# Performance work log

Hardware: AMD Instinct MI355X
Metric: run time of the kernel (lower is better)

Reference implementation:

```python
import jax, jax.numpy as jnp
import numpy as np

SLOPE = 25.0  # fast_sigmoid surrogate slope
BETA = 0.5    # leaky membrane decay

@jax.custom_vjp
def spike_fn(v):
    # heaviside(v) with fast_sigmoid surrogate gradient; v = mem - threshold
    return (v > 0).astype(v.dtype)

def _spike_fwd(v):
    return (v > 0).astype(v.dtype), v

def _spike_bwd(v, g):
    return (g / (SLOPE * jnp.abs(v) + 1.0) ** 2,)

spike_fn.defvjp(_spike_fwd, _spike_bwd)

def _snn_forward(x, Ws, thrs, num_steps):
    # x: [B, T, IN] (time_first=False) -> [T, B, IN]
    xt = jnp.transpose(x, (1, 0, 2))[:num_steps]
    B = x.shape[0]
    mems0 = tuple(jnp.zeros((B, W.shape[0]), x.dtype) for W in Ws)

    def step(mems, x_t):
        spk = x_t
        new = []
        for W, thr, m in zip(Ws, thrs, mems):
            cur = spk @ W.T  # Linear, bias=False (dropout = identity in eval mode)
            # snntorch Leaky, reset_mechanism='subtract': reset computed from
            # previous mem and detached (mem_reset), then mem = beta*mem + I - reset*thr
            reset = jax.lax.stop_gradient((m > thr).astype(cur.dtype))
            m = BETA * m + cur - reset * thr
            spk = spike_fn(m - thr)
            new.append(m)
        return tuple(new), (spk, new[-1])

    _, (spk_rec, mem_rec) = jax.lax.scan(step, mems0, xt)
    return spk_rec, mem_rec  # each [T, B, OUT]

def setup_inputs() -> dict:
    key = jax.random.key(0)
    ks = jax.random.split(key, 4)
    B, T, IN, H, OUT = 256, 100, 700, 1024, 20
    x = jax.random.uniform(ks[0], (B, T, IN), dtype=jnp.float32)
    s0 = 1.0 / np.sqrt(IN)
    s1 = 1.0 / np.sqrt(H)
    W0 = jax.random.uniform(ks[1], (H, IN), jnp.float32, -s0, s0)
    W1 = jax.random.uniform(ks[2], (H, H), jnp.float32, -s1, s1)
    W2 = jax.random.uniform(ks[3], (OUT, H), jnp.float32, -s1, s1)
    thr = jnp.float32(0.1)
    return {"x": x, "W0": W0, "W1": W1, "W2": W2,
            "thr0": thr, "thr1": thr, "thr2": thr, "num_steps": T}

def reference(x, W0, W1, W2, thr0, thr1, thr2, num_steps):
    return _snn_forward(x, (W0, W1, W2), (thr0, thr1, thr2), num_steps)
```

## Files before the change

kernel.cpp:

```cpp
#include <hip/hip_runtime.h>
#include <hip/hip_bf16.h>
#include <stdint.h>

#define BATCH   256
#define T_STEPS 100
#define IN_DIM  700
#define H_DIM   1024
#define OUT_DIM 20
#define TC      8
#define NCHUNK  13


__device__ __forceinline__ void lif_epilogue8(
    const float s[4][4], float thr,
    float* __restrict__ mstate, uint16_t* __restrict__ spk_bits,
    int b, int n0, int tbase, int tx, int ty, int ln)
{
    const int half = ty & 1;
    const int g = ty & 3;
    float m[4];
#pragma unroll
    for (int j = 0; j < 4; ++j)
        m[j] = mstate[(size_t)b * H_DIM + n0 + tx + 16 * j];
#pragma unroll
    for (int i = 0; i < 4; ++i) {
#pragma unroll
        for (int j = 0; j < 4; ++j) {
            const float rst = (m[j] > thr) ? thr : 0.f;
            float v = 0.5f * m[j] + s[i][j];
            v = v - rst; m[j] = v;
        }
        const int t = tbase + i;
#pragma unroll
        for (int j = 0; j < 4; ++j) {
            const unsigned long long mask = __ballot(m[j] > thr);
            if (tx == 0 && half == 0 && t < T_STEPS)
                spk_bits[((size_t)t * BATCH + b) * 64 + (n0 >> 4) + j] =
                    (uint16_t)((mask >> (16 * g)) & 0xFFFFull);
        }
    }
#pragma unroll
    for (int j = 0; j < 4; ++j)
        m[j] = __shfl(m[j], half ? (ln - 16) : ln);
#pragma unroll
    for (int i = 0; i < 4; ++i) {
#pragma unroll
        for (int j = 0; j < 4; ++j) {
            const float rst = (m[j] > thr) ? thr : 0.f;
            float v = 0.5f * m[j] + s[i][j];
            v = v - rst; m[j] = v;
        }
        const int t = tbase + 4 + i;
#pragma unroll
        for (int j = 0; j < 4; ++j) {
            const unsigned long long mask = __ballot(m[j] > thr);
            if (tx == 0 && half == 1 && t < T_STEPS)
                spk_bits[((size_t)t * BATCH + b) * 64 + (n0 >> 4) + j] =
                    (uint16_t)((mask >> (16 * g)) & 0xFFFFull);
        }
    }
    if (half == 1) {
#pragma unroll
        for (int j = 0; j < 4; ++j)
            mstate[(size_t)b * H_DIM + n0 + tx + 16 * j] = m[j];
    }
}

__global__ __launch_bounds__(256, 4) void fused_l0_l1(
    const float* __restrict__ x,
    const float* __restrict__ W0,
    const float* __restrict__ W1,
    const float* __restrict__ thr0_p,
    const float* __restrict__ thr1_p,
    float* __restrict__ m0state,
    float* __restrict__ m1state,
    uint16_t* __restrict__ spk0_bits,
    uint16_t* __restrict__ spk1_bits,
    int tc)
{
    __shared__ __align__(16) float As[64][68];
    __shared__ __align__(16) float Ws[64][68];

    const int tid = threadIdx.x;
    const int tx = tid & 15, ty = tid >> 4, ln = tid & 63;
    const int by = blockIdx.y;
    const bool isL0 = (blockIdx.x < 16);
    const int n0 = (isL0 ? blockIdx.x : blockIdx.x - 16) * 64;
    const int myc = isL0 ? tc : tc - 1;
    if (isL0 && myc >= NCHUNK) return;
    if (!isL0 && myc < 0) return;

    float ps[4][4], s[4][4];
#pragma unroll
    for (int i = 0; i < 4; ++i)
#pragma unroll
        for (int j = 0; j < 4; ++j) { ps[i][j] = 0.f; s[i][j] = 0.f; }

    const int sr = tid >> 2, q4 = tid & 3;
    const int b_s = 8 * by + (sr >> 3);
    int t_s = myc * TC + (sr & 7);
    if (t_s > T_STEPS - 1) t_s = T_STEPS - 1;
    const int b = 8 * by + (ty >> 1);

    if (isL0) {
        const float* xsrc = x + ((size_t)b_s * T_STEPS + t_s) * IN_DIM;
        const float* wsrc = W0 + (size_t)(n0 + sr) * IN_DIM;
#pragma unroll 1
        for (int c = 0; c < 11; ++c) {
            __syncthreads();
#pragma unroll
            for (int u = 0; u < 4; ++u) {
                const int f4 = q4 * 4 + u;
                const int k = c * 64 + f4 * 4;
                const float4 av = (k < IN_DIM) ? *(const float4*)(xsrc + k)
                                               : make_float4(0.f, 0.f, 0.f, 0.f);
                *(float4*)&As[sr][f4 * 4] = av;
                const float4 wv = (k < IN_DIM) ? *(const float4*)(wsrc + k)
                                               : make_float4(0.f, 0.f, 0.f, 0.f);
                *(float4*)&Ws[sr][f4 * 4] = wv;
            }
            __syncthreads();
            const int kmax4 = (c == 10) ? 15 : 16;
            for (int k4 = 0; k4 < kmax4; ++k4) {
                float4 av[4], wv[4];
#pragma unroll
                for (int i = 0; i < 4; ++i)
                    av[i] = *(const float4*)&As[4 * ty + i][k4 * 4];
#pragma unroll
                for (int j = 0; j < 4; ++j)
                    wv[j] = *(const float4*)&Ws[tx + 16 * j][k4 * 4];
#pragma unroll
                for (int i = 0; i < 4; ++i)
#pragma unroll
                    for (int j = 0; j < 4; ++j) {
                        ps[i][j] = __builtin_fmaf(av[i].x, wv[j].x, ps[i][j]);
                        ps[i][j] = __builtin_fmaf(av[i].y, wv[j].y, ps[i][j]);
                        ps[i][j] = __builtin_fmaf(av[i].z, wv[j].z, ps[i][j]);
                        ps[i][j] = __builtin_fmaf(av[i].w, wv[j].w, ps[i][j]);
                    }
            }
            if (c == 7 || c == 10) {
#pragma unroll
                for (int i = 0; i < 4; ++i)
#pragma unroll
                    for (int j = 0; j < 4; ++j) { s[i][j] += ps[i][j]; ps[i][j] = 0.f; }
            }
        }
        lif_epilogue8(s, *thr0_p, m0state, spk0_bits, b, n0, myc * TC, tx, ty, ln);
    } else {
        const uint16_t* bsrc = spk0_bits + ((size_t)t_s * BATCH + b_s) * 64;
        const float* wsrc = W1 + (size_t)(n0 + sr) * H_DIM;
#pragma unroll 1
        for (int c = 0; c < 16; ++c) {
            __syncthreads();
            {
                const uint32_t w = bsrc[c * 4 + q4];
#pragma unroll
                for (int u = 0; u < 4; ++u) {
                    float4 v;
                    v.x = ((w >> (u * 4 + 0)) & 1u) ? 1.0f : 0.0f;
                    v.y = ((w >> (u * 4 + 1)) & 1u) ? 1.0f : 0.0f;
                    v.z = ((w >> (u * 4 + 2)) & 1u) ? 1.0f : 0.0f;
                    v.w = ((w >> (u * 4 + 3)) & 1u) ? 1.0f : 0.0f;
                    *(float4*)&As[sr][(q4 * 4 + u) * 4] = v;
                }
#pragma unroll
                for (int u = 0; u < 4; ++u) {
                    const int f4 = q4 * 4 + u;
                    const float4 wv = *(const float4*)(wsrc + c * 64 + f4 * 4);
                    *(float4*)&Ws[sr][f4 * 4] = wv;
                }
            }
            __syncthreads();
            for (int k4 = 0; k4 < 16; ++k4) {
                float4 av[4], wv[4];
#pragma unroll
                for (int i = 0; i < 4; ++i)
                    av[i] = *(const float4*)&As[4 * ty + i][k4 * 4];
#pragma unroll
                for (int j = 0; j < 4; ++j)
                    wv[j] = *(const float4*)&Ws[tx + 16 * j][k4 * 4];
#pragma unroll
                for (int i = 0; i < 4; ++i)
#pragma unroll
                    for (int j = 0; j < 4; ++j) {
                        ps[i][j] = __builtin_fmaf(av[i].x, wv[j].x, ps[i][j]);
                        ps[i][j] = __builtin_fmaf(av[i].y, wv[j].y, ps[i][j]);
                        ps[i][j] = __builtin_fmaf(av[i].z, wv[j].z, ps[i][j]);
                        ps[i][j] = __builtin_fmaf(av[i].w, wv[j].w, ps[i][j]);
                    }
            }
            if (c == 7 || c == 15) {
#pragma unroll
                for (int i = 0; i < 4; ++i)
#pragma unroll
                    for (int j = 0; j < 4; ++j) { s[i][j] += ps[i][j]; ps[i][j] = 0.f; }
            }
        }
        lif_epilogue8(s, *thr1_p, m1state, spk1_bits, b, n0, myc * TC, tx, ty, ln);
    }
}

__global__ __launch_bounds__(256) void k2a_gemm(
    const uint16_t* __restrict__ spk1_bits,
    const float* __restrict__ W2,
    float* __restrict__ cur2h)
{
    const int gid = blockIdx.x * 256 + threadIdx.x;
    const int grp = gid / 25600;
    const int q   = gid % 25600;
    const int nq  = grp >> 1;
    const int h   = grp & 1;

    const uint16_t* bits = spk1_bits + (size_t)q * 64 + h * 32;
    const float* wr0 = W2 + (size_t)(nq * 4 + 0) * H_DIM + h * 512;
    const float* wr1 = W2 + (size_t)(nq * 4 + 1) * H_DIM + h * 512;
    const float* wr2 = W2 + (size_t)(nq * 4 + 2) * H_DIM + h * 512;
    const float* wr3 = W2 + (size_t)(nq * 4 + 3) * H_DIM + h * 512;

    float ps[4] = {0.f, 0.f, 0.f, 0.f};
    for (int wi = 0; wi < 32; ++wi) {
        const uint32_t bw = bits[wi];
        const int kb = wi * 16;
#pragma unroll
        for (int f = 0; f < 4; ++f) {
            const float4 a = *(const float4*)(wr0 + kb + f * 4);
            const float4 bq = *(const float4*)(wr1 + kb + f * 4);
            const float4 cq = *(const float4*)(wr2 + kb + f * 4);
            const float4 dq = *(const float4*)(wr3 + kb + f * 4);
            const int base = f * 4;
            ps[0] += ((bw >> (base + 0)) & 1u) ? a.x : 0.f;
            ps[1] += ((bw >> (base + 0)) & 1u) ? bq.x : 0.f;
            ps[2] += ((bw >> (base + 0)) & 1u) ? cq.x : 0.f;
            ps[3] += ((bw >> (base + 0)) & 1u) ? dq.x : 0.f;
            ps[0] += ((bw >> (base + 1)) & 1u) ? a.y : 0.f;
            ps[1] += ((bw >> (base + 1)) & 1u) ? bq.y : 0.f;
            ps[2] += ((bw >> (base + 1)) & 1u) ? cq.y : 0.f;
            ps[3] += ((bw >> (base + 1)) & 1u) ? dq.y : 0.f;
            ps[0] += ((bw >> (base + 2)) & 1u) ? a.z : 0.f;
            ps[1] += ((bw >> (base + 2)) & 1u) ? bq.z : 0.f;
            ps[2] += ((bw >> (base + 2)) & 1u) ? cq.z : 0.f;
            ps[3] += ((bw >> (base + 2)) & 1u) ? dq.z : 0.f;
            ps[0] += ((bw >> (base + 3)) & 1u) ? a.w : 0.f;
            ps[1] += ((bw >> (base + 3)) & 1u) ? bq.w : 0.f;
            ps[2] += ((bw >> (base + 3)) & 1u) ? cq.w : 0.f;
            ps[3] += ((bw >> (base + 3)) & 1u) ? dq.w : 0.f;
        }
    }
    float* dst = cur2h + ((size_t)h * 25600 + q) * OUT_DIM + nq * 4;
#pragma unroll
    for (int j = 0; j < 4; ++j) dst[j] = ps[j];
}

__global__ __launch_bounds__(256) void k2b_lif_out(
    const float* __restrict__ cur2h,
    const float* __restrict__ thr_p,
    float* __restrict__ out)
{
    const int idx = blockIdx.x * 256 + threadIdx.x;
    if (idx >= BATCH * OUT_DIM) return;
    const float thr = *thr_p;
    const size_t stride = (size_t)BATCH * OUT_DIM;
    float m = 0.f;
    for (int t = 0; t < T_STEPS; ++t) {
        const float h0 = cur2h[(size_t)t * stride + idx];
        const float h1 = cur2h[(size_t)25600 * OUT_DIM + (size_t)t * stride + idx];
        const float cur = h0 + h1;
        const float rst = (m > thr) ? thr : 0.f;
        float v = 0.5f * m + cur;
        v = v - rst;
        m = v;
        out[(size_t)t * stride + idx] = (v > thr) ? 1.0f : 0.0f;
        out[(size_t)T_STEPS * stride + (size_t)t * stride + idx] = v;
    }
}

extern "C" void kernel_launch(void* const* d_in, const int* in_sizes, int n_in,
                              void* d_out, int out_size, void* d_ws, size_t ws_size,
                              hipStream_t stream)
{
    const float* x    = (const float*)d_in[0];
    const float* W0   = (const float*)d_in[1];
    const float* W1   = (const float*)d_in[2];
    const float* W2   = (const float*)d_in[3];
    const float* thr0 = (const float*)d_in[4];
    const float* thr1 = (const float*)d_in[5];
    const float* thr2 = (const float*)d_in[6];

    uint16_t* spk0_bits = (uint16_t*)d_ws;
    uint16_t* spk1_bits = spk0_bits + (size_t)T_STEPS * BATCH * 64;
    float*    cur2h     = (float*)(spk1_bits + (size_t)T_STEPS * BATCH * 64);
    float*    m0state   = cur2h + (size_t)2 * 25600 * OUT_DIM;
    float*    m1state   = m0state + (size_t)BATCH * H_DIM;

    hipMemsetAsync(m0state, 0, (size_t)BATCH * H_DIM * 2 * sizeof(float), stream);

    const dim3 grid(32, 32);
    for (int tc = 0; tc <= NCHUNK; ++tc)
        fused_l0_l1<<<grid, 256, 0, stream>>>(
            x, W0, W1, thr0, thr1, m0state, m1state, spk0_bits, spk1_bits, tc);

    k2a_gemm<<<1000, 256, 0, stream>>>(spk1_bits, W2, cur2h);
    k2b_lif_out<<<(BATCH * OUT_DIM + 255) / 256, 256, 0, stream>>>(
        cur2h, thr2, (float*)d_out);
}
```

Baseline: 1.799 ms.

## Double-buffer shared tiles with register prefetch and interleave L0/L1 blocks

Splits the K-loop into 32-wide chunks held in two shared-memory buffers, prefetching the next chunk's global data into registers while the current chunk is computed. This drops one barrier per iteration and overlaps global loads with FMAs. Layer-0 and layer-1 blocks are now interleaved by blockIdx parity rather than split into contiguous ranges, which evens out work across CUs. It adds register pressure and doubles the number of loop iterations.

```diff
diff --git a/kernel.cpp b/kernel.cpp
--- a/kernel.cpp
+++ b/kernel.cpp
@@ -9,6 +9,8 @@
 #define OUT_DIM 20
 #define TC      8
 #define NCHUNK  13
+#define L0_NC   22
+#define L1_NC   32
 
 
 __device__ __forceinline__ void lif_epilogue8(
@@ -78,14 +80,14 @@
     uint16_t* __restrict__ spk1_bits,
     int tc)
 {
-    __shared__ __align__(16) float As[64][68];
-    __shared__ __align__(16) float Ws[64][68];
+    __shared__ __align__(16) float As[2][64][36];
+    __shared__ __align__(16) float Ws[2][64][36];
 
     const int tid = threadIdx.x;
     const int tx = tid & 15, ty = tid >> 4, ln = tid & 63;
     const int by = blockIdx.y;
-    const bool isL0 = (blockIdx.x < 16);
-    const int n0 = (isL0 ? blockIdx.x : blockIdx.x - 16) * 64;
+    const bool isL0 = ((blockIdx.x & 1) == 0);
+    const int n0 = (blockIdx.x >> 1) * 64;
     const int myc = isL0 ? tc : tc - 1;
     if (isL0 && myc >= NCHUNK) return;
     if (!isL0 && myc < 0) return;
@@ -105,30 +107,43 @@
     if (isL0) {
         const float* xsrc = x + ((size_t)b_s * T_STEPS + t_s) * IN_DIM;
         const float* wsrc = W0 + (size_t)(n0 + sr) * IN_DIM;
+        float4 pfa[2], pfw[2];
+#pragma unroll
+        for (int u = 0; u < 2; ++u) {
+            const int k = (q4 * 2 + u) * 4;
+            pfa[u] = (k < IN_DIM) ? *(const float4*)(xsrc + k)
+                                  : make_float4(0.f, 0.f, 0.f, 0.f);
+            pfw[u] = (k < IN_DIM) ? *(const float4*)(wsrc + k)
+                                  : make_float4(0.f, 0.f, 0.f, 0.f);
+        }
+        int cur = 0;
 #pragma unroll 1
-        for (int c = 0; c < 11; ++c) {
+        for (int c = 0; c < L0_NC; ++c) {
+#pragma unroll
+            for (int u = 0; u < 2; ++u) {
+                *(float4*)&As[cur][sr][(q4 * 2 + u) * 4] = pfa[u];
+                *(float4*)&Ws[cur][sr][(q4 * 2 + u) * 4] = pfw[u];
+            }
+            if (c + 1 < L0_NC) {
+#pragma unroll
+                for (int u = 0; u < 2; ++u) {
+                    const int k = (c + 1) * 32 + (q4 * 2 + u) * 4;
+                    pfa[u] = (k < IN_DIM) ? *(const float4*)(xsrc + k)
+                                          : make_float4(0.f, 0.f, 0.f, 0.f);
+                    pfw[u] = (k < IN_DIM) ? *(const float4*)(wsrc + k)
+                                          : make_float4(0.f, 0.f, 0.f, 0.f);
+                }
+            }
             __syncthreads();
-#pragma unroll
-            for (int u = 0; u < 4; ++u) {
-                const int f4 = q4 * 4 + u;
-                const int k = c * 64 + f4 * 4;
-                const float4 av = (k < IN_DIM) ? *(const float4*)(xsrc + k)
-                                               : make_float4(0.f, 0.f, 0.f, 0.f);
-                *(float4*)&As[sr][f4 * 4] = av;
-                const float4 wv = (k < IN_DIM) ? *(const float4*)(wsrc + k)
-                                               : make_float4(0.f, 0.f, 0.f, 0.f);
-                *(float4*)&Ws[sr][f4 * 4] = wv;
-            }
-            __syncthreads();
-            const int kmax4 = (c == 10) ? 15 : 16;
+            const int kmax4 = (c == L0_NC - 1) ? 7 : 8;
             for (int k4 = 0; k4 < kmax4; ++k4) {
                 float4 av[4], wv[4];
 #pragma unroll
                 for (int i = 0; i < 4; ++i)
-                    av[i] = *(const float4*)&As[4 * ty + i][k4 * 4];
+                    av[i] = *(const float4*)&As[cur][4 * ty + i][k4 * 4];
 #pragma unroll
                 for (int j = 0; j < 4; ++j)
-                    wv[j] = *(const float4*)&Ws[tx + 16 * j][k4 * 4];
+                    wv[j] = *(const float4*)&Ws[cur][tx + 16 * j][k4 * 4];
 #pragma unroll
                 for (int i = 0; i < 4; ++i)
 #pragma unroll
@@ -139,47 +154,55 @@
                         ps[i][j] = __builtin_fmaf(av[i].w, wv[j].w, ps[i][j]);
                     }
             }
-            if (c == 7 || c == 10) {
+            if (c == 15 || c == L0_NC - 1) {
 #pragma unroll
                 for (int i = 0; i < 4; ++i)
 #pragma unroll
                     for (int j = 0; j < 4; ++j) { s[i][j] += ps[i][j]; ps[i][j] = 0.f; }
             }
+            cur ^= 1;
         }
         lif_epilogue8(s, *thr0_p, m0state, spk0_bits, b, n0, myc * TC, tx, ty, ln);
     } else {
         const uint16_t* bsrc = spk0_bits + ((size_t)t_s * BATCH + b_s) * 64;
         const float* wsrc = W1 + (size_t)(n0 + sr) * H_DIM;
+        uint32_t pfb;
+        float4 pfw[2];
+        pfb = (*(const uint32_t*)(bsrc)) >> (q4 * 8);
+#pragma unroll
+        for (int u = 0; u < 2; ++u)
+            pfw[u] = *(const float4*)(wsrc + (q4 * 2 + u) * 4);
+        int cur = 0;
 #pragma unroll 1
-        for (int c = 0; c < 16; ++c) {
-            __syncthreads();
+        for (int c = 0; c < L1_NC; ++c) {
             {
-                const uint32_t w = bsrc[c * 4 + q4];
-#pragma unroll
-                for (int u = 0; u < 4; ++u) {
+                const uint32_t w = pfb;
+#pragma unroll
+                for (int u = 0; u < 2; ++u) {
                     float4 v;
                     v.x = ((w >> (u * 4 + 0)) & 1u) ? 1.0f : 0.0f;
                     v.y = ((w >> (u * 4 + 1)) & 1u) ? 1.0f : 0.0f;
                     v.z = ((w >> (u * 4 + 2)) & 1u) ? 1.0f : 0.0f;
                     v.w = ((w >> (u * 4 + 3)) & 1u) ? 1.0f : 0.0f;
-                    *(float4*)&As[sr][(q4 * 4 + u) * 4] = v;
+                    *(float4*)&As[cur][sr][(q4 * 2 + u) * 4] = v;
+                    *(float4*)&Ws[cur][sr][(q4 * 2 + u) * 4] = pfw[u];
                 }
-#pragma unroll
-                for (int u = 0; u < 4; ++u) {
-                    const int f4 = q4 * 4 + u;
-                    const float4 wv = *(const float4*)(wsrc + c * 64 + f4 * 4);
-                    *(float4*)&Ws[sr][f4 * 4] = wv;
-                }
+            }
+            if (c + 1 < L1_NC) {
+                pfb = (*(const uint32_t*)(bsrc + (c + 1) * 2)) >> (q4 * 8);
+#pragma unroll
+                for (int u = 0; u < 2; ++u)
+                    pfw[u] = *(const float4*)(wsrc + (c + 1) * 32 + (q4 * 2 + u) * 4);
             }
             __syncthreads();
-            for (int k4 = 0; k4 < 16; ++k4) {
+            for (int k4 = 0; k4 < 8; ++k4) {
                 float4 av[4], wv[4];
 #pragma unroll
                 for (int i = 0; i < 4; ++i)
-                    av[i] = *(const float4*)&As[4 * ty + i][k4 * 4];
+                    av[i] = *(const float4*)&As[cur][4 * ty + i][k4 * 4];
 #pragma unroll
                 for (int j = 0; j < 4; ++j)
-                    wv[j] = *(const float4*)&Ws[tx + 16 * j][k4 * 4];
+                    wv[j] = *(const float4*)&Ws[cur][tx + 16 * j][k4 * 4];
 #pragma unroll
                 for (int i = 0; i < 4; ++i)
 #pragma unroll
@@ -190,12 +213,13 @@
                         ps[i][j] = __builtin_fmaf(av[i].w, wv[j].w, ps[i][j]);
                     }
             }
-            if (c == 7 || c == 15) {
+            if (c == 15 || c == L1_NC - 1) {
 #pragma unroll
                 for (int i = 0; i < 4; ++i)
 #pragma unroll
                     for (int j = 0; j < 4; ++j) { s[i][j] += ps[i][j]; ps[i][j] = 0.f; }
             }
+            cur ^= 1;
         }
         lif_epilogue8(s, *thr1_p, m1state, spk1_bits, b, n0, myc * TC, tx, ty, ln);
     }
```

After: 2.501 ms. +39.1%, slower.
